# Optimization experiments

Measured on AMD Instinct MI355X. Metric: run time of the kernel, lower is better.

Reference implementation:

```python
import jax, jax.numpy as jnp
import numpy as np
import math

N, K, M = 4, 2048, 1024   # batch, seq_len, dim_in
DQ, DV = 1024, 1024       # dim_q, dim_v


def _xavier_uniform(k, shape, fan_in, fan_out):
    bound = math.sqrt(6.0 / (fan_in + fan_out))
    return jax.random.uniform(k, shape, jnp.float32, -bound, bound)


def setup_inputs() -> dict:
    key = jax.random.key(0)
    ks = jax.random.split(key, 9)
    query = jax.random.normal(ks[0], (N, K, M), jnp.float32)
    key_t = jax.random.normal(ks[1], (N, K, M), jnp.float32)
    value = jax.random.normal(ks[2], (N, K, M), jnp.float32)
    # causal mask: True above diagonal -> masked out (typical production usage)
    mask = jnp.broadcast_to(jnp.triu(jnp.ones((K, K), bool), k=1), (N, K, K))
    Wq = _xavier_uniform(ks[3], (DQ, M), M, DQ)
    bq = jax.random.uniform(ks[4], (DQ,), jnp.float32, -1 / math.sqrt(M), 1 / math.sqrt(M))
    Wk = _xavier_uniform(ks[5], (DQ, M), M, DQ)
    bk = jax.random.uniform(ks[6], (DQ,), jnp.float32, -1 / math.sqrt(M), 1 / math.sqrt(M))
    Wv = _xavier_uniform(ks[7], (DV, M), M, DV)
    bv = jax.random.uniform(ks[8], (DV,), jnp.float32, -1 / math.sqrt(M), 1 / math.sqrt(M))
    return {"query": query, "key": key_t, "value": value, "mask": mask,
            "Wq": Wq, "bq": bq, "Wk": Wk, "bk": bk, "Wv": Wv, "bv": bv}


def reference(query, key, value, mask, Wq, bq, Wk, bk, Wv, bv):
    # linear projections (torch Linear: x @ W.T + b)
    Q = jnp.einsum("nkm,dm->nkd", query, Wq) + bq   # (N, K, DQ)
    Kp = jnp.einsum("nkm,dm->nkd", key, Wk) + bk    # (N, K, DQ)
    V = jnp.einsum("nkm,dm->nkd", value, Wv) + bv   # (N, K, DV)
    # scaled dot product; scale uses projected dim (dim_q)
    scores = jnp.einsum("nqd,nkd->nqk", Q, Kp) / jnp.sqrt(jnp.float32(DQ))
    scores = jnp.where(mask, jnp.float32(-1e9), scores)
    w = jax.nn.softmax(scores, axis=2)               # (N, K, K)
    y = jnp.einsum("nqk,nkd->nqd", w, V)             # (N, K, DV)
    return y
```

## Files before the change

kernel.cpp:

```cpp
#include <hip/hip_runtime.h>
#include <hip/hip_bf16.h>


typedef __bf16 bf16x8 __attribute__((ext_vector_type(8)));
typedef float  f32x4  __attribute__((ext_vector_type(4)));

#define BM 128
#define BN 128
#define BKK 64

__device__ __forceinline__ int swz(int row, int slot) {
    return row * 128 + (((slot) ^ (row & 7)) << 4);
}

__device__ __forceinline__ void gload16(const __bf16* g, __bf16* l) {
    __builtin_amdgcn_global_load_lds((const __attribute__((address_space(1))) void*)g,
                                     (__attribute__((address_space(3))) void*)l, 16, 0, 0);
}

__device__ __forceinline__ void xcd_remap(int& bx, int& by, int& bz) {
    const int nx = gridDim.x, ny = gridDim.y;
    const int nwg = nx * ny * gridDim.z;
    const int flat = blockIdx.x + nx * (blockIdx.y + ny * blockIdx.z);
    const int q = nwg >> 3, r = nwg & 7;
    const int xcd = flat & 7, idx = flat >> 3;
    const int l = (xcd < r ? xcd * (q + 1) : r * (q + 1) + (xcd - r) * q) + idx;
    bx = l % nx; by = (l / nx) % ny; bz = l / (nx * ny);
}

__global__ __launch_bounds__(256)
void gemm_projb(const __bf16* __restrict__ Xb, const __bf16* __restrict__ Wb,
                const float* __restrict__ b0, const float* __restrict__ b1,
                const float* __restrict__ b2, float scaleQ,
                __bf16* __restrict__ QKV, __bf16* __restrict__ Vt)
{
    __shared__ char smem[65536];
    __bf16* smA = (__bf16*)smem;
    __bf16* smB = (__bf16*)(smem + 32768);

    int bx, by, bz;
    xcd_remap(bx, by, bz);
    const int m0 = by * BM, n0 = bx * BN;
    const int z = bz;
    const __bf16* Az = Xb + (long)z * 8388608L;
    const __bf16* Bz = Wb + (long)z * 1048576L;

    const int tid = threadIdx.x;
    const int wid = tid >> 6, lane = tid & 63;
    const int wm = (wid >> 1) * 64, wn = (wid & 1) * 64;
    const int g = lane >> 4, li = lane & 15;
    const int rl = lane >> 3;
    const int sg = (lane & 7) ^ rl;

    f32x4 acc[4][4];
#pragma unroll
    for (int i = 0; i < 4; i++)
#pragma unroll
        for (int j = 0; j < 4; j++)
            acc[i][j] = (f32x4){0.f, 0.f, 0.f, 0.f};

    auto STAGE = [&](int buf, int k0) {
#pragma unroll
        for (int i = 0; i < 4; i++) {
            const int seg = i * 4 + wid;
            const int r = seg * 8 + rl;
            gload16(Az + (long)(m0 + r) * 1024 + k0 + sg * 8, smA + buf * 8192 + seg * 512);
            gload16(Bz + (long)(n0 + r) * 1024 + k0 + sg * 8, smB + buf * 8192 + seg * 512);
        }
    };

    auto COMPUTE = [&](int buf) {
        const char* bA = (const char*)(smA + buf * 8192);
        const char* bB = (const char*)(smB + buf * 8192);
#pragma unroll
        for (int kk = 0; kk < 2; kk++) {
            const int slot = kk * 4 + g;
            bf16x8 af[4], bfv[4];
#pragma unroll
            for (int t = 0; t < 4; t++)
                af[t] = *(const bf16x8*)(bA + swz(wm + t * 16 + li, slot));
#pragma unroll
            for (int t = 0; t < 4; t++)
                bfv[t] = *(const bf16x8*)(bB + swz(wn + t * 16 + li, slot));
#pragma unroll
            for (int tm = 0; tm < 4; tm++)
#pragma unroll
                for (int tn = 0; tn < 4; tn++)
                    acc[tm][tn] = __builtin_amdgcn_mfma_f32_16x16x32_bf16(
                        af[tm], bfv[tn], acc[tm][tn], 0, 0, 0);
        }
    };

    const int nt = 16;
    STAGE(0, 0);
    __syncthreads();
    int cur = 0;
    for (int t = 0; t < nt - 1; ++t) {
        STAGE(cur ^ 1, (t + 1) * BKK);
        COMPUTE(cur);
        __syncthreads();
        cur ^= 1;
    }
    COMPUTE(cur);

    if (z < 2) {
        const float scale = (z == 0) ? scaleQ : 1.f;
        const float* bias = (z == 0) ? b0 : b1;
        __bf16* C = QKV + (long)z * 8388608L;
#pragma unroll
        for (int tm = 0; tm < 4; tm++)
#pragma unroll
            for (int tn = 0; tn < 4; tn++) {
                const int row = m0 + wm + tm * 16 + g * 4;
                const int col = n0 + wn + tn * 16 + li;
                const float b = bias[col];
#pragma unroll
                for (int j = 0; j < 4; j++)
                    C[(long)(row + j) * 1024 + col] = (__bf16)((acc[tm][tn][j] + b) * scale);
            }
    } else {
        __syncthreads();
        __bf16* T = (__bf16*)smem;
#pragma unroll
        for (int tm = 0; tm < 4; tm++)
#pragma unroll
            for (int tn = 0; tn < 4; tn++) {
                const int rowl = wm + tm * 16 + g * 4;
                const int coll = wn + tn * 16 + li;
                const float b = b2[n0 + coll];
#pragma unroll
                for (int j = 0; j < 4; j++)
                    T[coll * 136 + rowl + j] = (__bf16)(acc[tm][tn][j] + b);
            }
        __syncthreads();
        const long nb = m0 >> 11;
        const int kbase = m0 & 2047;
        __bf16* Vtb = Vt + nb * 2097152L;
#pragma unroll
        for (int it = 0; it < 8; it++) {
            const int lin = tid + 256 * it;
            const int c = lin >> 4;
            const int r0 = (lin & 15) * 8;
            bf16x8 v = *(const bf16x8*)(T + c * 136 + r0);
            *(bf16x8*)(Vtb + (long)(n0 + c) * 2048 + kbase + r0) = v;
        }
    }
}

template<int MODE>
__global__ __launch_bounds__(256)
void gemm_bt(const __bf16* __restrict__ Ap, const __bf16* __restrict__ Bp,
             void* __restrict__ Cp, int Kd, int lda, int ldb, int ldc,
             long strideA, long strideB, long strideC)
{
    __shared__ __bf16 smA[2][BM * BKK];
    __shared__ __bf16 smB[2][BN * BKK];

    int bx, by, bz;
    xcd_remap(bx, by, bz);

    const int tid = threadIdx.x;
    const int m0 = by * BM;
    const int n0 = bx * BN;
    if (MODE == 1 && n0 > m0) return;

    const long z = bz;
    int kEnd = Kd;
    if (MODE == 2) { int lim = m0 + BM; kEnd = lim < Kd ? lim : Kd; }

    const int wid = tid >> 6, lane = tid & 63;
    const int wm = (wid >> 1) * 64, wn = (wid & 1) * 64;
    const int g = lane >> 4, li = lane & 15;
    const int rl = lane >> 3;
    const int sg = (lane & 7) ^ rl;
    const __bf16* Az = Ap + z * strideA;
    const __bf16* Bz = Bp + z * strideB;

    f32x4 acc[4][4];
    for (int i = 0; i < 4; i++)
        for (int j = 0; j < 4; j++)
            acc[i][j] = (f32x4){0.f, 0.f, 0.f, 0.f};

    auto STAGE = [&](int buf, int k0) {
        for (int i = 0; i < 4; i++) {
            const int seg = i * 4 + wid;
            const int r = seg * 8 + rl;
            gload16(Az + (long)(m0 + r) * lda + k0 + sg * 8, &smA[buf][seg * 512]);
            gload16(Bz + (long)(n0 + r) * ldb + k0 + sg * 8, &smB[buf][seg * 512]);
        }
    };

    auto COMPUTE = [&](int buf) {
        for (int kk = 0; kk < 2; kk++) {
            const int slot = kk * 4 + g;
            bf16x8 af[4], bfv[4];
            for (int t = 0; t < 4; t++)
                af[t] = *(const bf16x8*)((const char*)&smA[buf][0] + swz(wm + t * 16 + li, slot));
            for (int t = 0; t < 4; t++)
                bfv[t] = *(const bf16x8*)((const char*)&smB[buf][0] + swz(wn + t * 16 + li, slot));
            for (int tm = 0; tm < 4; tm++)
                for (int tn = 0; tn < 4; tn++)
                    acc[tm][tn] = __builtin_amdgcn_mfma_f32_16x16x32_bf16(
                        af[tm], bfv[tn], acc[tm][tn], 0, 0, 0);
        }
    };

    const int nt = kEnd / BKK;
    STAGE(0, 0);
    __syncthreads();
    int cur = 0;
    for (int t = 0; t < nt - 1; ++t) {
        STAGE(cur ^ 1, (t + 1) * BKK);
        COMPUTE(cur);
        __syncthreads();
        cur ^= 1;
    }
    COMPUTE(cur);

    for (int tm = 0; tm < 4; tm++) {
        for (int tn = 0; tn < 4; tn++) {
            const int row = m0 + wm + tm * 16 + g * 4;
            const int col = n0 + wn + tn * 16 + li;
            float* C = (float*)Cp + z * strideC;
            for (int j = 0; j < 4; j++)
                C[(long)(row + j) * ldc + col] = acc[tm][tn][j];
        }
    }
}

__global__ __launch_bounds__(256)
void cvt3(const float* __restrict__ s0, const float* __restrict__ s1,
          const float* __restrict__ s2, __bf16* __restrict__ d0,
          __bf16* __restrict__ d1, __bf16* __restrict__ d2, long n)
{
    const int zz = blockIdx.y;
    const float* src = zz == 0 ? s0 : (zz == 1 ? s1 : s2);
    __bf16* dst = zz == 0 ? d0 : (zz == 1 ? d1 : d2);
    long i = ((long)blockIdx.x * 256 + threadIdx.x) * 8;
    const long stride = (long)gridDim.x * 2048;
    for (; i < n; i += stride) {
        float4 a = *(const float4*)(src + i);
        float4 b = *(const float4*)(src + i + 4);
        bf16x8 v;
        v[0] = (__bf16)a.x; v[1] = (__bf16)a.y; v[2] = (__bf16)a.z; v[3] = (__bf16)a.w;
        v[4] = (__bf16)b.x; v[5] = (__bf16)b.y; v[6] = (__bf16)b.z; v[7] = (__bf16)b.w;
        *(bf16x8*)(dst + i) = v;
    }
}

__global__ __launch_bounds__(256)
void softmax_causal(float* __restrict__ S)
{
    const int q = blockIdx.x;
    const long rowoff = (long)blockIdx.y * 2048 + q;
    const float* Srow = S + rowoff * 2048;
    __bf16* Prow = (__bf16*)S + rowoff * 4096;

    const int tid = threadIdx.x;
    const int wid = tid >> 6, lane = tid & 63;
    const int ni = ((q | 127) + 256) >> 8;

    float v[8];
    float mx = -1e30f;
    for (int i = 0; i < ni; i++) {
        int idx = tid + 256 * i;
        v[i] = (idx <= q) ? Srow[idx] : -1e30f;
        mx = fmaxf(mx, v[i]);
    }
    for (int off = 32; off; off >>= 1) mx = fmaxf(mx, __shfl_xor(mx, off));
    __shared__ float red[8];
    if (lane == 0) red[wid] = mx;
    __syncthreads();
    mx = fmaxf(fmaxf(red[0], red[1]), fmaxf(red[2], red[3]));

    float e[8];
    float s = 0.f;
    for (int i = 0; i < ni; i++) {
        int idx = tid + 256 * i;
        e[i] = (idx <= q) ? __expf(v[i] - mx) : 0.f;
        s += e[i];
    }
    for (int off = 32; off; off >>= 1) s += __shfl_xor(s, off);
    if (lane == 0) red[4 + wid] = s;
    __syncthreads();
    s = red[4] + red[5] + red[6] + red[7];
    const float inv = 1.f / s;

    const int qc = q | 127;
    for (int i = 0; i < ni; i++) {
        int idx = tid + 256 * i;
        if (idx <= qc) Prow[idx] = (__bf16)(e[i] * inv);
    }
}

extern "C" void kernel_launch(void* const* d_in, const int* in_sizes, int n_in,
                              void* d_out, int out_size, void* d_ws, size_t ws_size,
                              hipStream_t stream) {
    const float* query = (const float*)d_in[0];
    const float* key   = (const float*)d_in[1];
    const float* value = (const float*)d_in[2];
    const float* Wq = (const float*)d_in[4];
    const float* bq = (const float*)d_in[5];
    const float* Wk = (const float*)d_in[6];
    const float* bk = (const float*)d_in[7];
    const float* Wv = (const float*)d_in[8];
    const float* bv = (const float*)d_in[9];
    float* out = (float*)d_out;

    char* ws = (char*)d_ws;
    const long MB = 1L << 20;
    __bf16* QKV = (__bf16*)(ws);
    __bf16* Vt  = (__bf16*)(ws + 48 * MB);
    float*  S   = (float*) (ws + 64 * MB);
    __bf16* Xb  = (__bf16*)(ws + 64 * MB);
    __bf16* Wb  = (__bf16*)(ws + 112 * MB);

    const dim3 blk(256);
    const long nX = 2048L * 1024 * 4;
    const long nW = 1024L * 1024;

    cvt3<<<dim3(1024, 3), blk, 0, stream>>>(query, key, value,
        Xb, Xb + 8388608L, Xb + 2 * 8388608L, nX);
    cvt3<<<dim3(512, 3), blk, 0, stream>>>(Wq, Wk, Wv,
        Wb, Wb + 1048576L, Wb + 2 * 1048576L, nW);

    gemm_projb<<<dim3(8, 64, 3), blk, 0, stream>>>(
        Xb, Wb, bq, bk, bv, 1.f / 32.f, QKV, Vt);

    gemm_bt<1><<<dim3(16, 16, 4), blk, 0, stream>>>(QKV, QKV + 8388608L, S,
        1024, 1024, 1024, 2048, 2048L * 1024, 2048L * 1024, 2048L * 2048);

    softmax_causal<<<dim3(2048, 4), blk, 0, stream>>>(S);

    gemm_bt<2><<<dim3(8, 16, 4), blk, 0, stream>>>((__bf16*)S, Vt, out,
        2048, 4096, 2048, 1024, 2048L * 4096, 1024L * 2048, 2048L * 1024);
}
```

Before: 191.4 us.

## Merge conversion launches, swizzle V-transpose LDS, rebalance causal PV tile order

Folds the two fp32-to-bf16 conversion launches into one six-slice kernel to cut launch overhead and the tail of the smaller launch. Adds an XOR swizzle to the LDS staging buffer used for the V transpose, aiming to reduce bank conflicts on the strided writes. Also permutes row-block order in the causal PV GEMM so blocks with long and short k-ranges are interleaved, for better load balance. The weight-conversion slices now launch 1024 blocks, most of which exit without work.

```diff
diff --git a/kernel.cpp b/kernel.cpp
--- a/kernel.cpp
+++ b/kernel.cpp
@@ -128,9 +128,10 @@
                 const int rowl = wm + tm * 16 + g * 4;
                 const int coll = wn + tn * 16 + li;
                 const float b = b2[n0 + coll];
+                const int rsw = rowl ^ ((coll & 7) << 4);
 #pragma unroll
                 for (int j = 0; j < 4; j++)
-                    T[coll * 136 + rowl + j] = (__bf16)(acc[tm][tn][j] + b);
+                    T[coll * 136 + rsw + j] = (__bf16)(acc[tm][tn][j] + b);
             }
         __syncthreads();
         const long nb = m0 >> 11;
@@ -141,7 +142,7 @@
             const int lin = tid + 256 * it;
             const int c = lin >> 4;
             const int r0 = (lin & 15) * 8;
-            bf16x8 v = *(const bf16x8*)(T + c * 136 + r0);
+            bf16x8 v = *(const bf16x8*)(T + c * 136 + (r0 ^ ((c & 7) << 4)));
             *(bf16x8*)(Vtb + (long)(n0 + c) * 2048 + kbase + r0) = v;
         }
     }
@@ -158,6 +159,12 @@
 
     int bx, by, bz;
     xcd_remap(bx, by, bz);
+
+    if (MODE == 2) {
+        const int t = by >> 2, r = by & 3;
+        by = (t == 0) ? by : (t == 1) ? 19 - by : (t == 2) ? by - 4 : 23 - by;
+        (void)r;
+    }
 
     const int tid = threadIdx.x;
     const int m0 = by * BM;
@@ -229,13 +236,17 @@
 }
 
 __global__ __launch_bounds__(256)
-void cvt3(const float* __restrict__ s0, const float* __restrict__ s1,
-          const float* __restrict__ s2, __bf16* __restrict__ d0,
-          __bf16* __restrict__ d1, __bf16* __restrict__ d2, long n)
+void cvt6(const float* __restrict__ s0, const float* __restrict__ s1,
+          const float* __restrict__ s2, const float* __restrict__ s3,
+          const float* __restrict__ s4, const float* __restrict__ s5,
+          __bf16* __restrict__ dX, __bf16* __restrict__ dW)
 {
-    const int zz = blockIdx.y;
-    const float* src = zz == 0 ? s0 : (zz == 1 ? s1 : s2);
-    __bf16* dst = zz == 0 ? d0 : (zz == 1 ? d1 : d2);
+    const int y = blockIdx.y;
+    const float* src = y == 0 ? s0 : y == 1 ? s1 : y == 2 ? s2
+                     : y == 3 ? s3 : y == 4 ? s4 : s5;
+    const long n = (y < 3) ? 8388608L : 1048576L;
+    __bf16* dst = (y < 3) ? dX + (long)y * 8388608L : dW + (long)(y - 3) * 1048576L;
+
     long i = ((long)blockIdx.x * 256 + threadIdx.x) * 8;
     const long stride = (long)gridDim.x * 2048;
     for (; i < n; i += stride) {
@@ -316,13 +327,8 @@
     __bf16* Wb  = (__bf16*)(ws + 112 * MB);
 
     const dim3 blk(256);
-    const long nX = 2048L * 1024 * 4;
-    const long nW = 1024L * 1024;
-
-    cvt3<<<dim3(1024, 3), blk, 0, stream>>>(query, key, value,
-        Xb, Xb + 8388608L, Xb + 2 * 8388608L, nX);
-    cvt3<<<dim3(512, 3), blk, 0, stream>>>(Wq, Wk, Wv,
-        Wb, Wb + 1048576L, Wb + 2 * 1048576L, nW);
+
+    cvt6<<<dim3(1024, 6), blk, 0, stream>>>(query, key, value, Wq, Wk, Wv, Xb, Wb);
 
     gemm_projb<<<dim3(8, 64, 3), blk, 0, stream>>>(
         Xb, Wb, bq, bk, bv, 1.f / 32.f, QKV, Vt);
```

New measurement: 189.5 us. About the same (-1.0%).
